# Optimization experiments

Measured on AMD Instinct MI355X. Metric: run time of the kernel, lower is better.

## Reference

```python
import jax, jax.numpy as jnp
import numpy as np

EMBED_DIM = 64
D_STATE = 16
D_CONV = 4
EXPAND = 2
DT_RANK = 8
D_INNER = EXPAND * EMBED_DIM  # 128
B_, T_, H_, W_ = 4, 16, 16, 16


def _causal_dwconv(x, w, b):
    # x: (B, D, L), w: (D, 1, K) depthwise causal conv (left pad K-1), matches
    # torch conv1d(padding=K-1)[..., :L]
    K = w.shape[-1]
    y = jax.lax.conv_general_dilated(
        x, w, window_strides=(1,), padding=[(K - 1, 0)],
        feature_group_count=x.shape[1], dimension_numbers=('NCH', 'OIH', 'NCH'))
    return y + b[None, :, None]


def _selective_scan(u, delta, A, Bm, Cm, D):
    # u, delta: (B, d, L); A: (d, n); Bm, Cm: (B, n, L); D: (d,)
    dA = jnp.exp(jnp.einsum('bdl,dn->lbdn', delta, A))      # (L,B,d,n)
    dBu = jnp.einsum('bdl,bnl,bdl->lbdn', delta, Bm, u)     # (L,B,d,n)
    h0 = jnp.zeros(dA.shape[1:], dA.dtype)

    def step(h, xs):
        dA_t, dBu_t = xs
        h = dA_t * h + dBu_t
        return h, h

    _, hs = jax.lax.scan(step, h0, (dA, dBu))               # (L,B,d,n)
    y = jnp.einsum('lbdn,bnl->bdl', hs, Cm)
    return y + u * D[None, :, None]


def _mamba_branch(x, z, conv_w, conv_b, xproj_w, dtproj_w, dtproj_b, A_log, D):
    # x, z: (B, d_inner, L)
    x = jax.nn.silu(_causal_dwconv(x, conv_w, conv_b))
    x_dbl = jnp.einsum('bdl,ed->bel', x, xproj_w)           # e = dt_rank + 2*n
    dt = x_dbl[:, :DT_RANK]
    Bm = x_dbl[:, DT_RANK:DT_RANK + D_STATE]
    Cm = x_dbl[:, DT_RANK + D_STATE:]
    delta = jax.nn.softplus(jnp.einsum('brl,dr->bdl', dt, dtproj_w) + dtproj_b[None, :, None])
    A = -jnp.exp(A_log)
    y = _selective_scan(x, delta, A, Bm, Cm, D)
    return y * jax.nn.silu(z)


def _conv3d(x, w, b, pad):
    y = jax.lax.conv_general_dilated(
        x, w, window_strides=(1, 1, 1), padding=[(pad, pad)] * 3,
        dimension_numbers=('NCDHW', 'OIDHW', 'NCDHW'))
    return y + b[None, :, None, None, None]


def setup_inputs() -> dict:
    key = jax.random.key(0)
    ks = jax.random.split(key, 24)
    s = 0.02
    d, n, r, K, C = D_INNER, D_STATE, DT_RANK, D_CONV, EMBED_DIM
    inp = {
        'x': jax.random.normal(ks[0], (B_, C, T_, H_, W_), jnp.float32),
        'in_proj_w': jax.random.normal(ks[1], (2 * d, C), jnp.float32) * s,
        'conv_w': jax.random.normal(ks[2], (d, 1, K), jnp.float32) * s,
        'conv_b': jnp.zeros((d,), jnp.float32),
        'xproj_w': jax.random.normal(ks[3], (r + 2 * n, d), jnp.float32) * s,
        'dtproj_w': jax.random.normal(ks[4], (d, r), jnp.float32) * s,
        'dtproj_b': jax.random.normal(ks[5], (d,), jnp.float32) * s,
        'A_log': jnp.tile(jnp.log(jnp.arange(1, n + 1, dtype=jnp.float32))[None, :], (d, 1)),
        'D': jnp.ones((d,), jnp.float32),
        'conv_w_b': jax.random.normal(ks[6], (d, 1, K), jnp.float32) * s,
        'conv_b_b': jnp.zeros((d,), jnp.float32),
        'xproj_w_b': jax.random.normal(ks[7], (r + 2 * n, d), jnp.float32) * s,
        'dtproj_w_b': jax.random.normal(ks[8], (d, r), jnp.float32) * s,
        'dtproj_b_b': jax.random.normal(ks[9], (d,), jnp.float32) * s,
        'A_b_log': jnp.tile(jnp.log(jnp.arange(1, n + 1, dtype=jnp.float32))[None, :], (d, 1)),
        'D_b': jnp.ones((d,), jnp.float32),
        'out_proj_w': jax.random.normal(ks[10], (C, d), jnp.float32) * s,
        'proj_w': jax.random.normal(ks[11], (C, C, 3, 3, 3), jnp.float32) * s,
        'proj_b': jnp.zeros((C,), jnp.float32),
        'norm_w': jax.random.normal(ks[12], (C, C, 1, 1, 1), jnp.float32) * s,
        'norm_b': jnp.zeros((C,), jnp.float32),
    }
    return inp


def reference(x, in_proj_w, conv_w, conv_b, xproj_w, dtproj_w, dtproj_b, A_log, D,
              conv_w_b, conv_b_b, xproj_w_b, dtproj_w_b, dtproj_b_b, A_b_log, D_b,
              out_proj_w, proj_w, proj_b, norm_w, norm_b):
    residual = x
    B, C, T, H, W = x.shape
    # SpectralPriority scan: b c t h w -> b c (h w t)
    seq = x.transpose(0, 1, 3, 4, 2).reshape(B, C, H * W * T)
    # bimamba v2
    xz = jnp.einsum('bcl,ec->bel', seq, in_proj_w)          # (B, 2*d_inner, L)
    x_f, z_f = xz[:, :D_INNER], xz[:, D_INNER:]
    y_f = _mamba_branch(x_f, z_f, conv_w, conv_b, xproj_w, dtproj_w, dtproj_b, A_log, D)
    xz_r = jnp.flip(xz, -1)
    x_b, z_b = xz_r[:, :D_INNER], xz_r[:, D_INNER:]
    y_b = _mamba_branch(x_b, z_b, conv_w_b, conv_b_b, xproj_w_b, dtproj_w_b, dtproj_b_b, A_b_log, D_b)
    out = y_f + jnp.flip(y_b, -1)                           # (B, d_inner, L)
    out = jnp.einsum('bdl,cd->blc', out, out_proj_w)        # (B, L, C)
    x_recon = out.reshape(B, C, T, H, W)
    x3 = _conv3d(x_recon, proj_w, proj_b, pad=1)
    return _conv3d(x3 + residual, norm_w, norm_b, pad=0)
```

## Files before the change

kernel.cpp:

```cpp
#include <hip/hip_runtime.h>


#define NL 4096

typedef unsigned short u16;
typedef unsigned int u32;
typedef __attribute__((ext_vector_type(8))) short bf16x8;
typedef __attribute__((ext_vector_type(4))) float f32x4;

__device__ __forceinline__ float siluf_(float x) {
  return x * __builtin_amdgcn_rcpf(1.f + __expf(-x));
}
__device__ __forceinline__ float softplusf_(float x) {
  return (x > 20.f) ? x : __logf(1.f + __expf(x));
}
__device__ __forceinline__ u16 f2bf(float f) {
  u32 u = __float_as_uint(f);
  u += 0x7fffu + ((u >> 16) & 1u);
  return (u16)(u >> 16);
}
__device__ __forceinline__ float bflo(u32 v) { return __uint_as_float(v << 16); }
__device__ __forceinline__ float bfhi(u32 v) { return __uint_as_float(v & 0xFFFF0000u); }

__device__ __forceinline__ float rowsum16_(float p) {
  int q;
  q = __builtin_amdgcn_mov_dpp(__float_as_int(p), 0x121, 0xf, 0xf, false);
  p += __int_as_float(q);
  q = __builtin_amdgcn_mov_dpp(__float_as_int(p), 0x122, 0xf, 0xf, false);
  p += __int_as_float(q);
  q = __builtin_amdgcn_mov_dpp(__float_as_int(p), 0x124, 0xf, 0xf, false);
  p += __int_as_float(q);
  q = __builtin_amdgcn_mov_dpp(__float_as_int(p), 0x128, 0xf, 0xf, false);
  p += __int_as_float(q);
  return p;
}

#define OXZ  0u
#define OUCF 1048576u
#define OUCB 1572864u
#define ODLF 2424832u
#define ODLB 2949120u
#define OYF  3473408u
#define OYB  3997696u
#define OO   4521984u
#define OO2  5046272u
#define PER_B 5570560u

#define NCH 64
#define CL  64
#define WB1 110592u

__global__ __launch_bounds__(256) void kxz(
    const float* __restrict__ x, const float* __restrict__ wip,
    float* __restrict__ ws, int b0) {
  int bi = blockIdx.y, gb = b0 + bi;
  float* s = ws + (size_t)bi * PER_B;
  int bid = blockIdx.x;
  int h = bid >> 4, w = bid & 15;
  int tid = threadIdx.x;
  __shared__ float xs[64][16];
  for (int i = tid; i < 1024; i += 256) {
    int c = i >> 4, t = i & 15;
    xs[c][t] = x[(size_t)(gb * 64 + c) * NL + t * 256 + h * 16 + w];
  }
  __syncthreads();
  int e = tid;
  float acc[16];
#pragma unroll
  for (int t = 0; t < 16; ++t) acc[t] = 0.f;
  for (int c = 0; c < 64; ++c) {
    float wv = wip[e * 64 + c];
#pragma unroll
    for (int t = 0; t < 16; ++t) acc[t] = fmaf(wv, xs[c][t], acc[t]);
  }
  float4* dst = (float4*)(s + OXZ + (size_t)e * NL + h * 256 + w * 16);
#pragma unroll
  for (int q = 0; q < 4; ++q)
    dst[q] = make_float4(acc[q * 4], acc[q * 4 + 1], acc[q * 4 + 2], acc[q * 4 + 3]);
}

__global__ __launch_bounds__(256) void k2prep(
    const float* __restrict__ cwf, const float* __restrict__ cbf,
    const float* __restrict__ xpf, const float* __restrict__ dtwf,
    const float* __restrict__ dtbf,
    const float* __restrict__ cwb, const float* __restrict__ cbb,
    const float* __restrict__ xpb, const float* __restrict__ dtwb,
    const float* __restrict__ dtbb,
    float* __restrict__ ws) {
  int bi = blockIdx.y;
  float* s = ws + (size_t)bi * PER_B;
  int bx = blockIdx.x;
  int lt = bx >> 1, dir = bx & 1;
  int l0 = lt * 32;
  int lout0 = dir ? (127 - lt) * 32 : l0;
  int tid = threadIdx.x;

  __shared__ float pool[128 * 40];
  __shared__ u16 uct[32][136];
  float (*X)[40] = (float(*)[40])pool;

  for (int i = tid; i < 128 * 38; i += 256) {
    int d = i / 38, j = i - d * 38;
    int l = l0 - 3 + j;
    X[d][j] = (l >= 0 && l < NL) ? s[OXZ + (size_t)d * NL + l] : 0.f;
  }
  __syncthreads();

  const float* cw = dir ? cwb : cwf;
  const float* cb = dir ? cbb : cbf;
  u16* ucg = (u16*)(s + (dir ? OUCB : OUCF));
  for (int i = tid; i < 128 * 32; i += 256) {
    int d = i >> 5, li = i & 31;
    float a = cb[d];
    if (dir == 0) {
#pragma unroll
      for (int k = 0; k < 4; ++k) a = fmaf(cw[d * 4 + k], X[d][li + k], a);
    } else {
#pragma unroll
      for (int k = 0; k < 4; ++k) a = fmaf(cw[d * 4 + k], X[d][37 - li - k], a);
    }
    a = siluf_(a);
    u16 ab = f2bf(a);
    uct[li][d] = ab;
    ucg[(size_t)d * NL + lout0 + li] = ab;
  }
  __syncthreads();

  float* xds = pool;
  {
    int wid = tid >> 6, lane = tid & 63;
    int n16 = lane & 15, kg = lane >> 4;
    const float* xp = dir ? xpb : xpf;
#pragma unroll
    for (int rep = 0; rep < 2; ++rep) {
      int id = wid + rep * 4;
      if (id < 6) {
        int et = id >> 1, lt2 = id & 1;
        f32x4 acc = {};
#pragma unroll
        for (int ks = 0; ks < 4; ++ks) {
          bf16x8 bfrag = *(const bf16x8*)&uct[lt2 * 16 + n16][ks * 32 + kg * 8];
          int e = et * 16 + n16;
          int ec = (e < 40) ? e : 39;
          const float* pa = xp + ec * 128 + ks * 32 + kg * 8;
          float4 a0 = *(const float4*)pa;
          float4 a1 = *(const float4*)(pa + 4);
          bf16x8 af;
          af[0] = (short)f2bf(a0.x); af[1] = (short)f2bf(a0.y);
          af[2] = (short)f2bf(a0.z); af[3] = (short)f2bf(a0.w);
          af[4] = (short)f2bf(a1.x); af[5] = (short)f2bf(a1.y);
          af[6] = (short)f2bf(a1.z); af[7] = (short)f2bf(a1.w);
          acc = __builtin_amdgcn_mfma_f32_16x16x32_bf16(af, bfrag, acc, 0, 0, 0);
        }
#pragma unroll
        for (int rg = 0; rg < 4; ++rg) {
          int e = et * 16 + kg * 4 + rg;
          if (e < 40) xds[e * 33 + lt2 * 16 + n16] = acc[rg];
        }
      }
    }
  }
  __syncthreads();

  const float* dtw = dir ? dtwb : dtwf;
  const float* dtb = dir ? dtbb : dtbf;
  u16* dlg = (u16*)(s + (dir ? ODLB : ODLF));
  for (int i = tid; i < 128 * 32; i += 256) {
    int d = i >> 5, li = i & 31;
    float pre = dtb[d];
#pragma unroll
    for (int r = 0; r < 8; ++r)
      pre = fmaf(dtw[d * 8 + r], xds[r * 33 + li], pre);
    dlg[(size_t)d * NL + lout0 + li] = f2bf(softplusf_(pre));
  }
  u16* bctp = (u16*)(s + OO2);
  for (int i = tid; i < 32 * 32; i += 256) {
    int li = i >> 5, k = i & 31;
    bctp[((size_t)dir * 4096 + lout0 + li) * 32 + k] = f2bf(xds[(8 + k) * 33 + li]);
  }
}

__global__ __launch_bounds__(256) void kscanA(
    const float* __restrict__ Alf, const float* __restrict__ Alb,
    float* __restrict__ ws) {
  int bi = blockIdx.y;
  float* s = ws + (size_t)bi * PER_B;
  int xid = blockIdx.x;
  int chunk = xid >> 4, dir = (xid >> 3) & 1, d8 = xid & 7;
  int tid = threadIdx.x;
  int wv = tid >> 6, lane = tid & 63;
  int n = lane & 15, g = lane >> 4;
  int d = d8 * 16 + wv * 4 + g;
  int l0 = chunk * CL;
  __shared__ float bl[CL * 32];
  {
    const u16* bctp = (const u16*)(s + OO2) + ((size_t)dir * 4096 + l0) * 32;
    for (int i = tid; i < CL * 32; i += 256)
      bl[i] = __uint_as_float(((u32)bctp[i]) << 16);
  }
  __syncthreads();
  const u16* ucp = (const u16*)(s + (dir ? OUCB : OUCF)) + (size_t)d * NL + l0;
  const u16* dlp = (const u16*)(s + (dir ? ODLB : ODLF)) + (size_t)d * NL + l0;
  float A = -__expf((dir ? Alb : Alf)[d * 16 + n]);
  float P = 1.f, S = 0.f;
  for (int i0 = 0; i0 < CL; i0 += 8) {
    uint4 dq = *(const uint4*)(dlp + i0);
    uint4 uq = *(const uint4*)(ucp + i0);
    float dv[8] = {bflo(dq.x), bfhi(dq.x), bflo(dq.y), bfhi(dq.y),
                   bflo(dq.z), bfhi(dq.z), bflo(dq.w), bfhi(dq.w)};
    float uv[8] = {bflo(uq.x), bfhi(uq.x), bflo(uq.y), bfhi(uq.y),
                   bflo(uq.z), bfhi(uq.z), bflo(uq.w), bfhi(uq.w)};
#pragma unroll
    for (int j = 0; j < 8; ++j) {
      float dA = __expf(dv[j] * A);
      S = fmaf(dA, S, dv[j] * bl[(i0 + j) * 32 + n] * uv[j]);
      P *= dA;
    }
  }
  size_t cidx = ((size_t)(chunk * 2 + dir) * 128 + d) * 16 + n;
  s[OO + cidx] = P;
  s[OO + 262144u + cidx] = S;
}

__global__ __launch_bounds__(64) void kscanB(float* __restrict__ ws) {
  int bi = blockIdx.y;
  float* s = ws + (size_t)bi * PER_B;
  int dir = blockIdx.x >> 5, dblk = blockIdx.x & 31;
  int tid = threadIdx.x;
  size_t base = (size_t)dir * 2048 + dblk * 64 + tid;
  float carry = 0.f;
#pragma unroll 4
  for (int c = 0; c < NCH; ++c) {
    size_t idx = (size_t)c * 4096 + base;
    float pv = s[OO + idx], sv = s[OO + 262144u + idx];
    s[OO + 262144u + idx] = carry;
    carry = fmaf(pv, carry, sv);
  }
}

__global__ __launch_bounds__(256) void kscanC(
    const float* __restrict__ Alf, const float* __restrict__ Df,
    const float* __restrict__ Alb, const float* __restrict__ Db,
    float* __restrict__ ws) {
  int bi = blockIdx.y;
  float* s = ws + (size_t)bi * PER_B;
  int xid = blockIdx.x;
  int chunk = xid >> 4, dir = (xid >> 3) & 1, d8 = xid & 7;
  int tid = threadIdx.x;
  int wv = tid >> 6, lane = tid & 63;
  int n = lane & 15, g = lane >> 4;
  int d = d8 * 16 + wv * 4 + g;
  int l0 = chunk * CL;
  __shared__ float bl[CL * 32];
  __shared__ float ps[16][65];
  {
    const u16* bctp = (const u16*)(s + OO2) + ((size_t)dir * 4096 + l0) * 32;
    for (int i = tid; i < CL * 32; i += 256)
      bl[i] = __uint_as_float(((u32)bctp[i]) << 16);
  }
  __syncthreads();
  const u16* ucp = (const u16*)(s + (dir ? OUCB : OUCF)) + (size_t)d * NL + l0;
  const u16* dlp = (const u16*)(s + (dir ? ODLB : ODLF)) + (size_t)d * NL + l0;
  float* ybase = s + (dir ? OYB : OYF);
  float A = -__expf((dir ? Alb : Alf)[d * 16 + n]);
  float Dv = (dir ? Db : Df)[d];
  size_t cidx = ((size_t)(chunk * 2 + dir) * 128 + d) * 16 + n;
  float h = s[OO + 262144u + cidx];
  int prow = wv * 4 + g;
  for (int i0 = 0; i0 < CL; i0 += 8) {
    uint4 dq = *(const uint4*)(dlp + i0);
    uint4 uq = *(const uint4*)(ucp + i0);
    float dv[8] = {bflo(dq.x), bfhi(dq.x), bflo(dq.y), bfhi(dq.y),
                   bflo(dq.z), bfhi(dq.z), bflo(dq.w), bfhi(dq.w)};
    float uv[8] = {bflo(uq.x), bfhi(uq.x), bflo(uq.y), bfhi(uq.y),
                   bflo(uq.z), bfhi(uq.z), bflo(uq.w), bfhi(uq.w)};
#pragma unroll
    for (int j = 0; j < 8; ++j) {
      int i = i0 + j;
      float dA = __expf(dv[j] * A);
      h = fmaf(dA, h, dv[j] * bl[i * 32 + n] * uv[j]);
      float p = rowsum16_(h * bl[i * 32 + 16 + n]);
      if (n == 0) ps[prow][i] = fmaf(uv[j], Dv, p);
    }
  }
  __syncthreads();
  for (int i = tid; i < 16 * CL; i += 256) {
    int row = i >> 6, col = i & 63;
    ybase[(size_t)(d8 * 16 + row) * NL + l0 + col] = ps[row][col];
  }
}

__global__ __launch_bounds__(256) void koutg(
    const float* __restrict__ wout, float* __restrict__ ws) {
  int bi = blockIdx.y;
  float* s = ws + (size_t)bi * PER_B;
  int lt = blockIdx.x;
  int l0 = lt * 32;
  int tid = threadIdx.x;
  __shared__ u16 otb[32][136];
  for (int i = tid; i < 128 * 32; i += 256) {
    int d = i >> 5, li = i & 31;
    int l = l0 + li;
    float z = s[OXZ + (size_t)(128 + d) * NL + l];
    float v = s[OYF + (size_t)d * NL + l] + s[OYB + (size_t)d * NL + (NL - 1 - l)];
    otb[li][d] = f2bf(v * siluf_(z));
  }
  __syncthreads();
  int wid = tid >> 6, lane = tid & 63;
  int n16 = lane & 15, kg = lane >> 4;
  f32x4 acc[2] = {};
  const float* wr = wout + (size_t)(wid * 16 + n16) * 128 + kg * 8;
#pragma unroll
  for (int ks = 0; ks < 4; ++ks) {
    const float* pa = wr + ks * 32;
    float4 a0 = *(const float4*)pa;
    float4 a1 = *(const float4*)(pa + 4);
    bf16x8 af;
    af[0] = (short)f2bf(a0.x); af[1] = (short)f2bf(a0.y);
    af[2] = (short)f2bf(a0.z); af[3] = (short)f2bf(a0.w);
    af[4] = (short)f2bf(a1.x); af[5] = (short)f2bf(a1.y);
    af[6] = (short)f2bf(a1.z); af[7] = (short)f2bf(a1.w);
    bf16x8 b0 = *(const bf16x8*)&otb[n16][ks * 32 + kg * 8];
    bf16x8 b1 = *(const bf16x8*)&otb[16 + n16][ks * 32 + kg * 8];
    acc[0] = __builtin_amdgcn_mfma_f32_16x16x32_bf16(af, b0, acc[0], 0, 0, 0);
    acc[1] = __builtin_amdgcn_mfma_f32_16x16x32_bf16(af, b1, acc[1], 0, 0, 0);
  }
#pragma unroll
  for (int l2 = 0; l2 < 2; ++l2) {
    float4 st = make_float4(acc[l2][0], acc[l2][1], acc[l2][2], acc[l2][3]);
    *(float4*)&s[OO2 + (size_t)(l0 + l2 * 16 + n16) * 64 + wid * 16 + kg * 4] = st;
  }
}

__global__ __launch_bounds__(256) void kprepw(
    const float* __restrict__ pw, float* __restrict__ wdst) {
  int off = blockIdx.x;
  u16* wb = (u16*)wdst;
  int tid = threadIdx.x;
  for (int i = tid; i < 4096; i += 256) {
    int co = i >> 6, ci = i & 63;
    u16 v = f2bf(pw[(size_t)(co * 64 + ci) * 27 + off]);
#pragma unroll
    for (int xc = 0; xc < 8; ++xc)
      wb[(size_t)xc * WB1 + off * 4096 + i] = v;
  }
}

__global__ __launch_bounds__(256, 1) void kconv3(
    const float* __restrict__ pb, const float* __restrict__ nw,
    const float* __restrict__ nb, const float* __restrict__ xin,
    float* __restrict__ out, const u16* __restrict__ wb,
    float* __restrict__ ws, int b0) {
  int bi = blockIdx.y, gb = b0 + bi;
  float* s = ws + (size_t)bi * PER_B;
  int bx = blockIdx.x;
  int t = bx >> 2, hq = bx & 3;
  int h0 = hq * 4;
  int tid = threadIdx.x;
  const float* xr = s + OO2;

  __shared__ u16 Xs[3 * 6 * 18 * 72];
  float* cx = (float*)Xs;
  {
    u32* xz32 = (u32*)Xs;
    for (int i = tid; i < 3 * 6 * 18 * 72 / 2; i += 256) xz32[i] = 0u;
  }
  __syncthreads();
  {
    int ci = tid >> 2, wq = tid & 3;
    for (int row = 0; row < 18; ++row) {
      int tt = row / 6, hh = row - tt * 6;
      int ts = t + tt - 1, hs = h0 + hh - 1;
      if (ts < 0 || ts > 15 || hs < 0 || hs > 15) continue;
      float4 v = *(const float4*)(xr + (size_t)ci * NL + ts * 256 + hs * 16 + wq * 4);
      int rb = (tt * 6 + hh) * 18 + 1 + wq * 4;
      Xs[(rb + 0) * 72 + ci] = f2bf(v.x);
      Xs[(rb + 1) * 72 + ci] = f2bf(v.y);
      Xs[(rb + 2) * 72 + ci] = f2bf(v.z);
      Xs[(rb + 3) * 72 + ci] = f2bf(v.w);
    }
  }
  __syncthreads();

  int wid = tid >> 6, lane = tid & 63;
  int cq = wid;
  int n16 = lane & 15, kg = lane >> 4;
  f32x4 acc[4] = {};

  const u16* wbA = wb + (size_t)(bx & 7) * WB1 +
                   (size_t)(cq * 16 + n16) * 64 + kg * 8;
#pragma unroll
  for (int kt = 0; kt < 3; ++kt)
#pragma unroll
    for (int kh = 0; kh < 3; ++kh) {
#pragma unroll
      for (int kw = 0; kw < 3; ++kw) {
        int off = (kt * 3 + kh) * 3 + kw;
        const u16* pa = wbA + off * 4096;
#pragma unroll
        for (int st = 0; st < 2; ++st) {
          int kb = st * 32;
          bf16x8 a0 = *(const bf16x8*)(pa + kb);
#pragma unroll
          for (int l2 = 0; l2 < 4; ++l2) {
            int r = (kt * 6 + l2 + kh) * 18 + n16 + kw;
            bf16x8 b0 = *(const bf16x8*)(&Xs[r * 72 + kb + kg * 8]);
            acc[l2] = __builtin_amdgcn_mfma_f32_16x16x32_bf16(a0, b0, acc[l2], 0, 0, 0);
          }
        }
      }
    }
  __syncthreads();

#pragma unroll
  for (int l2 = 0; l2 < 4; ++l2) {
    int lp = l2 * 16 + n16;
    int lg = t * 256 + (h0 + l2) * 16 + n16;
#pragma unroll
    for (int rg = 0; rg < 4; ++rg) {
      int co = cq * 16 + kg * 4 + rg;
      cx[co * 65 + lp] = acc[l2][rg] + pb[co] +
                         xin[(size_t)(gb * 64 + co) * NL + lg];
    }
  }
  __syncthreads();

  {
    int co2 = tid >> 2, pq = tid & 3;
    float mac[16];
#pragma unroll
    for (int j = 0; j < 16; ++j) mac[j] = 0.f;
    for (int ci = 0; ci < 64; ci += 4) {
      float4 w4 = *(const float4*)&nw[co2 * 64 + ci];
      float wv[4] = {w4.x, w4.y, w4.z, w4.w};
#pragma unroll
      for (int cc = 0; cc < 4; ++cc) {
        const float* row = &cx[(ci + cc) * 65 + pq * 16];
        float4 a = *(const float4*)&row[0];
        float4 b = *(const float4*)&row[4];
        float4 c = *(const float4*)&row[8];
        float4 e = *(const float4*)&row[12];
        mac[0] = fmaf(wv[cc], a.x, mac[0]);   mac[1] = fmaf(wv[cc], a.y, mac[1]);
        mac[2] = fmaf(wv[cc], a.z, mac[2]);   mac[3] = fmaf(wv[cc], a.w, mac[3]);
        mac[4] = fmaf(wv[cc], b.x, mac[4]);   mac[5] = fmaf(wv[cc], b.y, mac[5]);
        mac[6] = fmaf(wv[cc], b.z, mac[6]);   mac[7] = fmaf(wv[cc], b.w, mac[7]);
        mac[8] = fmaf(wv[cc], c.x, mac[8]);   mac[9] = fmaf(wv[cc], c.y, mac[9]);
        mac[10] = fmaf(wv[cc], c.z, mac[10]); mac[11] = fmaf(wv[cc], c.w, mac[11]);
        mac[12] = fmaf(wv[cc], e.x, mac[12]); mac[13] = fmaf(wv[cc], e.y, mac[13]);
        mac[14] = fmaf(wv[cc], e.z, mac[14]); mac[15] = fmaf(wv[cc], e.w, mac[15]);
      }
    }
    float bias = nb[co2];
    float4* dst = (float4*)(out + (size_t)(gb * 64 + co2) * NL +
                            t * 256 + h0 * 16 + pq * 16);
#pragma unroll
    for (int q = 0; q < 4; ++q)
      dst[q] = make_float4(mac[q * 4] + bias, mac[q * 4 + 1] + bias,
                           mac[q * 4 + 2] + bias, mac[q * 4 + 3] + bias);
  }
}

extern "C" void kernel_launch(void* const* d_in, const int* in_sizes, int n_in,
                              void* d_out, int out_size, void* d_ws, size_t ws_size,
                              hipStream_t stream) {
  const float* x    = (const float*)d_in[0];
  const float* wip  = (const float*)d_in[1];
  const float* cwf  = (const float*)d_in[2];
  const float* cbf  = (const float*)d_in[3];
  const float* xpf  = (const float*)d_in[4];
  const float* dtwf = (const float*)d_in[5];
  const float* dtbf = (const float*)d_in[6];
  const float* Alf  = (const float*)d_in[7];
  const float* Df   = (const float*)d_in[8];
  const float* cwb  = (const float*)d_in[9];
  const float* cbb  = (const float*)d_in[10];
  const float* xpb  = (const float*)d_in[11];
  const float* dtwb = (const float*)d_in[12];
  const float* dtbb = (const float*)d_in[13];
  const float* Alb  = (const float*)d_in[14];
  const float* Db   = (const float*)d_in[15];
  const float* wout = (const float*)d_in[16];
  const float* pw   = (const float*)d_in[17];
  const float* pb   = (const float*)d_in[18];
  const float* nw   = (const float*)d_in[19];
  const float* nb   = (const float*)d_in[20];

  const size_t PER_B_BYTES = (size_t)PER_B * 4;
  const size_t WB_BYTES = 8u * WB1 * 2u;
  int bcnt;
  if (ws_size >= 4 * PER_B_BYTES + WB_BYTES) bcnt = 4;
  else if (ws_size >= PER_B_BYTES + WB_BYTES) bcnt = 1;
  else return;
  int passes = 4 / bcnt;

  float* ws = (float*)d_ws;
  float* wsW = ws + (size_t)bcnt * PER_B;
  kprepw<<<dim3(27), 256, 0, stream>>>(pw, wsW);
  for (int p = 0; p < passes; ++p) {
    int b0 = p * bcnt;
    kxz   <<<dim3(256, bcnt), 256, 0, stream>>>(x, wip, ws, b0);
    k2prep<<<dim3(256, bcnt), 256, 0, stream>>>(cwf, cbf, xpf, dtwf, dtbf,
                                                cwb, cbb, xpb, dtwb, dtbb, ws);
    kscanA<<<dim3(1024, bcnt), 256, 0, stream>>>(Alf, Alb, ws);
    kscanB<<<dim3(64, bcnt), 64, 0, stream>>>(ws);
    kscanC<<<dim3(1024, bcnt), 256, 0, stream>>>(Alf, Df, Alb, Db, ws);
    koutg <<<dim3(128, bcnt), 256, 0, stream>>>(wout, ws);
    kconv3<<<dim3(64, bcnt), 256, 0, stream>>>(pb, nw, nb, x, (float*)d_out,
                                               (const u16*)wsW, ws, b0);
  }
}
```

Before: 260.6 us.

## Fold chunk carry scan into kscanC, shrink kscanA smem, split conv3 tiles finer

Removes the separate kscanB carry-propagation kernel. Each kscanC block now recomputes its starting state by serially combining the (P,S) pairs of all earlier chunks, which saves a launch and a serialized kernel at the cost of redundant global reads that grow with the chunk index. kscanA stages only the B half of the BC tile in shared memory. kconv3 now processes 2 h-rows per block instead of 4, doubling the grid to 128 blocks per batch, with smaller LDS and launch bounds that allow 2 blocks per CU, to improve occupancy and spread.

```diff
diff --git a/kernel.cpp b/kernel.cpp
--- a/kernel.cpp
+++ b/kernel.cpp
@@ -192,11 +192,13 @@
   int n = lane & 15, g = lane >> 4;
   int d = d8 * 16 + wv * 4 + g;
   int l0 = chunk * CL;
-  __shared__ float bl[CL * 32];
+  __shared__ float bl[CL * 16];
   {
     const u16* bctp = (const u16*)(s + OO2) + ((size_t)dir * 4096 + l0) * 32;
-    for (int i = tid; i < CL * 32; i += 256)
-      bl[i] = __uint_as_float(((u32)bctp[i]) << 16);
+    for (int i = tid; i < CL * 16; i += 256) {
+      int l = i >> 4, k = i & 15;
+      bl[i] = __uint_as_float(((u32)bctp[l * 32 + k]) << 16);
+    }
   }
   __syncthreads();
   const u16* ucp = (const u16*)(s + (dir ? OUCB : OUCF)) + (size_t)d * NL + l0;
@@ -213,29 +215,13 @@
 #pragma unroll
     for (int j = 0; j < 8; ++j) {
       float dA = __expf(dv[j] * A);
-      S = fmaf(dA, S, dv[j] * bl[(i0 + j) * 32 + n] * uv[j]);
+      S = fmaf(dA, S, dv[j] * bl[(i0 + j) * 16 + n] * uv[j]);
       P *= dA;
     }
   }
   size_t cidx = ((size_t)(chunk * 2 + dir) * 128 + d) * 16 + n;
   s[OO + cidx] = P;
   s[OO + 262144u + cidx] = S;
-}
-
-__global__ __launch_bounds__(64) void kscanB(float* __restrict__ ws) {
-  int bi = blockIdx.y;
-  float* s = ws + (size_t)bi * PER_B;
-  int dir = blockIdx.x >> 5, dblk = blockIdx.x & 31;
-  int tid = threadIdx.x;
-  size_t base = (size_t)dir * 2048 + dblk * 64 + tid;
-  float carry = 0.f;
-#pragma unroll 4
-  for (int c = 0; c < NCH; ++c) {
-    size_t idx = (size_t)c * 4096 + base;
-    float pv = s[OO + idx], sv = s[OO + 262144u + idx];
-    s[OO + 262144u + idx] = carry;
-    carry = fmaf(pv, carry, sv);
-  }
 }
 
 __global__ __launch_bounds__(256) void kscanC(
@@ -264,8 +250,16 @@
   float* ybase = s + (dir ? OYB : OYF);
   float A = -__expf((dir ? Alb : Alf)[d * 16 + n]);
   float Dv = (dir ? Db : Df)[d];
-  size_t cidx = ((size_t)(chunk * 2 + dir) * 128 + d) * 16 + n;
-  float h = s[OO + 262144u + cidx];
+  float h = 0.f;
+  {
+    size_t stepi = (size_t)d * 16 + n;
+#pragma unroll 4
+    for (int c = 0; c < chunk; ++c) {
+      size_t idx = ((size_t)(c * 2 + dir) * 128) * 16 + stepi;
+      float pv = s[OO + idx], sv = s[OO + 262144u + idx];
+      h = fmaf(pv, h, sv);
+    }
+  }
   int prow = wv * 4 + g;
   for (int i0 = 0; i0 < CL; i0 += 8) {
     uint4 dq = *(const uint4*)(dlp + i0);
@@ -346,7 +340,7 @@
   }
 }
 
-__global__ __launch_bounds__(256, 1) void kconv3(
+__global__ __launch_bounds__(256, 2) void kconv3(
     const float* __restrict__ pb, const float* __restrict__ nw,
     const float* __restrict__ nb, const float* __restrict__ xin,
     float* __restrict__ out, const u16* __restrict__ wb,
@@ -354,26 +348,27 @@
   int bi = blockIdx.y, gb = b0 + bi;
   float* s = ws + (size_t)bi * PER_B;
   int bx = blockIdx.x;
-  int t = bx >> 2, hq = bx & 3;
-  int h0 = hq * 4;
+  int t = bx >> 3, hq = bx & 7;
+  int h0 = hq * 2;
   int tid = threadIdx.x;
   const float* xr = s + OO2;
 
-  __shared__ u16 Xs[3 * 6 * 18 * 72];
+  __shared__ u16 Xs[3 * 4 * 18 * 72];
   float* cx = (float*)Xs;
   {
     u32* xz32 = (u32*)Xs;
-    for (int i = tid; i < 3 * 6 * 18 * 72 / 2; i += 256) xz32[i] = 0u;
+    for (int i = tid; i < 3 * 4 * 18 * 72 / 2; i += 256) xz32[i] = 0u;
   }
   __syncthreads();
   {
     int ci = tid >> 2, wq = tid & 3;
-    for (int row = 0; row < 18; ++row) {
-      int tt = row / 6, hh = row - tt * 6;
+#pragma unroll
+    for (int rowc = 0; rowc < 12; ++rowc) {
+      int tt = rowc >> 2, hh = rowc & 3;
       int ts = t + tt - 1, hs = h0 + hh - 1;
       if (ts < 0 || ts > 15 || hs < 0 || hs > 15) continue;
       float4 v = *(const float4*)(xr + (size_t)ci * NL + ts * 256 + hs * 16 + wq * 4);
-      int rb = (tt * 6 + hh) * 18 + 1 + wq * 4;
+      int rb = (tt * 4 + hh) * 18 + 1 + wq * 4;
       Xs[(rb + 0) * 72 + ci] = f2bf(v.x);
       Xs[(rb + 1) * 72 + ci] = f2bf(v.y);
       Xs[(rb + 2) * 72 + ci] = f2bf(v.z);
@@ -385,7 +380,7 @@
   int wid = tid >> 6, lane = tid & 63;
   int cq = wid;
   int n16 = lane & 15, kg = lane >> 4;
-  f32x4 acc[4] = {};
+  f32x4 acc[2] = {};
 
   const u16* wbA = wb + (size_t)(bx & 7) * WB1 +
                    (size_t)(cq * 16 + n16) * 64 + kg * 8;
@@ -402,8 +397,8 @@
           int kb = st * 32;
           bf16x8 a0 = *(const bf16x8*)(pa + kb);
 #pragma unroll
-          for (int l2 = 0; l2 < 4; ++l2) {
-            int r = (kt * 6 + l2 + kh) * 18 + n16 + kw;
+          for (int l2 = 0; l2 < 2; ++l2) {
+            int r = (kt * 4 + l2 + kh) * 18 + n16 + kw;
             bf16x8 b0 = *(const bf16x8*)(&Xs[r * 72 + kb + kg * 8]);
             acc[l2] = __builtin_amdgcn_mfma_f32_16x16x32_bf16(a0, b0, acc[l2], 0, 0, 0);
           }
@@ -413,13 +408,13 @@
   __syncthreads();
 
 #pragma unroll
-  for (int l2 = 0; l2 < 4; ++l2) {
+  for (int l2 = 0; l2 < 2; ++l2) {
     int lp = l2 * 16 + n16;
     int lg = t * 256 + (h0 + l2) * 16 + n16;
 #pragma unroll
     for (int rg = 0; rg < 4; ++rg) {
       int co = cq * 16 + kg * 4 + rg;
-      cx[co * 65 + lp] = acc[l2][rg] + pb[co] +
+      cx[co * 33 + lp] = acc[l2][rg] + pb[co] +
                          xin[(size_t)(gb * 64 + co) * NL + lg];
     }
   }
@@ -427,36 +422,28 @@
 
   {
     int co2 = tid >> 2, pq = tid & 3;
-    float mac[16];
-#pragma unroll
-    for (int j = 0; j < 16; ++j) mac[j] = 0.f;
+    float mac[8];
+#pragma unroll
+    for (int j = 0; j < 8; ++j) mac[j] = 0.f;
     for (int ci = 0; ci < 64; ci += 4) {
       float4 w4 = *(const float4*)&nw[co2 * 64 + ci];
       float wv[4] = {w4.x, w4.y, w4.z, w4.w};
 #pragma unroll
       for (int cc = 0; cc < 4; ++cc) {
-        const float* row = &cx[(ci + cc) * 65 + pq * 16];
+        const float* row = &cx[(ci + cc) * 33 + pq * 8];
         float4 a = *(const float4*)&row[0];
         float4 b = *(const float4*)&row[4];
-        float4 c = *(const float4*)&row[8];
-        float4 e = *(const float4*)&row[12];
-        mac[0] = fmaf(wv[cc], a.x, mac[0]);   mac[1] = fmaf(wv[cc], a.y, mac[1]);
-        mac[2] = fmaf(wv[cc], a.z, mac[2]);   mac[3] = fmaf(wv[cc], a.w, mac[3]);
-        mac[4] = fmaf(wv[cc], b.x, mac[4]);   mac[5] = fmaf(wv[cc], b.y, mac[5]);
-        mac[6] = fmaf(wv[cc], b.z, mac[6]);   mac[7] = fmaf(wv[cc], b.w, mac[7]);
-        mac[8] = fmaf(wv[cc], c.x, mac[8]);   mac[9] = fmaf(wv[cc], c.y, mac[9]);
-        mac[10] = fmaf(wv[cc], c.z, mac[10]); mac[11] = fmaf(wv[cc], c.w, mac[11]);
-        mac[12] = fmaf(wv[cc], e.x, mac[12]); mac[13] = fmaf(wv[cc], e.y, mac[13]);
-        mac[14] = fmaf(wv[cc], e.z, mac[14]); mac[15] = fmaf(wv[cc], e.w, mac[15]);
+        mac[0] = fmaf(wv[cc], a.x, mac[0]);  mac[1] = fmaf(wv[cc], a.y, mac[1]);
+        mac[2] = fmaf(wv[cc], a.z, mac[2]);  mac[3] = fmaf(wv[cc], a.w, mac[3]);
+        mac[4] = fmaf(wv[cc], b.x, mac[4]);  mac[5] = fmaf(wv[cc], b.y, mac[5]);
+        mac[6] = fmaf(wv[cc], b.z, mac[6]);  mac[7] = fmaf(wv[cc], b.w, mac[7]);
       }
     }
     float bias = nb[co2];
     float4* dst = (float4*)(out + (size_t)(gb * 64 + co2) * NL +
-                            t * 256 + h0 * 16 + pq * 16);
-#pragma unroll
-    for (int q = 0; q < 4; ++q)
-      dst[q] = make_float4(mac[q * 4] + bias, mac[q * 4 + 1] + bias,
-                           mac[q * 4 + 2] + bias, mac[q * 4 + 3] + bias);
+                            t * 256 + h0 * 16 + pq * 8);
+    dst[0] = make_float4(mac[0] + bias, mac[1] + bias, mac[2] + bias, mac[3] + bias);
+    dst[1] = make_float4(mac[4] + bias, mac[5] + bias, mac[6] + bias, mac[7] + bias);
   }
 }
 
@@ -502,10 +489,9 @@
     k2prep<<<dim3(256, bcnt), 256, 0, stream>>>(cwf, cbf, xpf, dtwf, dtbf,
                                                 cwb, cbb, xpb, dtwb, dtbb, ws);
     kscanA<<<dim3(1024, bcnt), 256, 0, stream>>>(Alf, Alb, ws);
-    kscanB<<<dim3(64, bcnt), 64, 0, stream>>>(ws);
     kscanC<<<dim3(1024, bcnt), 256, 0, stream>>>(Alf, Df, Alb, Db, ws);
     koutg <<<dim3(128, bcnt), 256, 0, stream>>>(wout, ws);
-    kconv3<<<dim3(64, bcnt), 256, 0, stream>>>(pb, nw, nb, x, (float*)d_out,
-                                               (const u16*)wsW, ws, b0);
-  }
-}
+    kconv3<<<dim3(128, bcnt), 256, 0, stream>>>(pb, nw, nb, x, (float*)d_out,
+                                                (const u16*)wsW, ws, b0);
+  }
+}
```

Measured after the change: 257.8 us. Within noise of the previous version (-1.1%).
